# Performance work log

Hardware: AMD Instinct MI355X
Metric: run time of the kernel (lower is better)

## Reference

```python
import jax, jax.numpy as jnp
import numpy as np

B, N, ND_, FEAT, WV = 32, 1024, 8, 2048, 300
E, T, STEPS = 20000, 2, 5
NDIM = N * ND_  # 8192


def setup_inputs() -> dict:
    key = jax.random.key(0)
    ks = jax.random.split(key, 20)
    s = 0.02
    inputs = jax.random.normal(ks[0], (B, FEAT), jnp.float32)
    wordvecs = jax.random.normal(ks[1], (N, WV), jnp.float32)
    # unique edges per type (disjoint across types) so the scatter has no duplicate indices
    rng = np.random.default_rng(0)
    codes = rng.permutation(N * N)[: T * E].reshape(T, E)
    edge_u = (codes // N).astype(np.int32)
    edge_v = (codes % N).astype(np.int32)
    ki = np.repeat(np.arange(ND_), ND_)
    kj = np.tile(np.arange(ND_), ND_)
    mat_u = (edge_u.reshape(-1)[:, None] * ND_ + ki[None, :]).reshape(-1).astype(np.int32)
    mat_v = (edge_v.reshape(-1)[:, None] * ND_ + kj[None, :]).reshape(-1).astype(np.int32)
    p = {
        'inputs': inputs, 'wordvecs': wordvecs,
        'edge_u': jnp.asarray(edge_u), 'edge_v': jnp.asarray(edge_v),
        'mat_u': jnp.asarray(mat_u), 'mat_v': jnp.asarray(mat_v),
        # Inputnet: Linear(feat+wv -> 512), Linear(512 -> node_dim)
        'W_in1': jax.random.normal(ks[2], (512, FEAT + WV), jnp.float32) * s,
        'b_in1': jnp.zeros((512,), jnp.float32),
        'W_in2': jax.random.normal(ks[3], (ND_, 512), jnp.float32) * s,
        'b_in2': jnp.zeros((ND_,), jnp.float32),
        # embnet: Linear(wv -> 50)
        'W_emb': jax.random.normal(ks[4], (50, WV), jnp.float32) * s,
        'b_emb': jnp.zeros((50,), jnp.float32),
        # relnets: one (50, 50*nd^2) matrix per edge type
        'rel_mats': jax.random.normal(ks[5], (T, 50, 50 * ND_ * ND_), jnp.float32) * s,
        # GRUCell(node_dim, node_dim)
        'W_ih': jax.random.normal(ks[6], (3 * ND_, ND_), jnp.float32) * s,
        'W_hh': jax.random.normal(ks[7], (3 * ND_, ND_), jnp.float32) * s,
        'b_ih': jnp.zeros((3 * ND_,), jnp.float32),
        'b_hh': jnp.zeros((3 * ND_,), jnp.float32),
        # outnet: Linear(nd -> 20), ReLU, Linear(20 -> 1)
        'W_o1': jax.random.normal(ks[8], (20, ND_), jnp.float32) * s,
        'b_o1': jnp.zeros((20,), jnp.float32),
        'W_o2': jax.random.normal(ks[9], (1, 20), jnp.float32) * s,
        'b_o2': jnp.zeros((1,), jnp.float32),
    }
    return p


def reference(inputs, wordvecs, edge_u, edge_v, mat_u, mat_v,
              W_in1, b_in1, W_in2, b_in2, W_emb, b_emb, rel_mats,
              W_ih, W_hh, b_ih, b_hh, W_o1, b_o1, W_o2, b_o2):
    nd = W_in2.shape[0]
    n_nodes = wordvecs.shape[0]
    ndim = n_nodes * nd
    bsz = inputs.shape[0]

    # Inputnet: per-(image, node) feature -> initial hidden state [B, N*nd]
    f = jnp.concatenate([
        jnp.broadcast_to(inputs[:, None, :], (bsz, n_nodes, inputs.shape[1])),
        jnp.broadcast_to(wordvecs[None, :, :], (bsz, n_nodes, wordvecs.shape[1])),
    ], axis=-1).reshape(bsz * n_nodes, -1)
    h = jax.nn.relu(f @ W_in1.T + b_in1) @ W_in2.T + b_in2  # [B*N, nd]
    hidden = h.reshape(bsz, ndim)

    # edge weights via Relnet per edge type
    embs = wordvecs @ W_emb.T + b_emb  # [N, 50]
    ws = []
    for t in range(rel_mats.shape[0]):
        ue = embs[edge_u[t]]  # [E, 50]
        ve = embs[edge_v[t]]  # [E, 50]
        tmp = (ue @ rel_mats[t]).reshape(ue.shape[0], embs.shape[1], nd * nd)
        ws.append(jnp.einsum('ed,edk->ek', ve, tmp))  # [E, nd^2]
    weights = jnp.concatenate(ws, axis=0).reshape(-1)

    # scatter into dense propagation matrix
    P = jnp.zeros((ndim, ndim), jnp.float32).at[mat_u, mat_v].set(weights)
    norm = jnp.sqrt(jnp.sum(P * P, axis=1))  # row L2 norms [ndim]
    norm = norm + (norm == 0).astype(P.dtype)
    P = P / norm  # NOTE: torch broadcasting divides COLUMNS by row norms (faithful)

    def gru(x, hc):
        gi = x @ W_ih.T + b_ih
        gh = hc @ W_hh.T + b_hh
        ir, iz, inn = jnp.split(gi, 3, axis=-1)
        hr, hz, hn = jnp.split(gh, 3, axis=-1)
        r = jax.nn.sigmoid(ir + hr)
        z = jax.nn.sigmoid(iz + hz)
        n = jnp.tanh(inn + r * hn)
        return (1.0 - z) * n + z * hc

    hiddens = [hidden]
    for _ in range(STEPS):
        x = jnp.tanh(hidden @ P.T)  # [B, ndim]
        hidden = gru(x.reshape(-1, nd), hidden.reshape(-1, nd)).reshape(bsz, ndim)
        hiddens.append(hidden)
    states = jnp.stack(hiddens, axis=1)  # [B, STEPS+1, ndim]

    o = jax.nn.relu(states.reshape(-1, nd) @ W_o1.T + b_o1) @ W_o2.T + b_o2  # [B*(S+1)*N, 1]
    logits = o.reshape(bsz, STEPS + 1, n_nodes).transpose(0, 2, 1)  # [B, N, S+1]
    return logits
```

## Files before the change

kernel.cpp:

```cpp
#include <hip/hip_runtime.h>
#include <math.h>

constexpr int B = 32, N = 1024, ND = 8, FEAT = 2048, WVD = 300;
constexpr int E = 20000, T = 2, STEPS = 5;
constexpr int NDIM = N * ND;
constexpr int H1 = 512;
constexpr int W1C = FEAT + WVD;
constexpr int EMB = 50;
constexpr int RC = EMB * ND * ND;
constexpr int SEG = 16;
constexpr int SEGLEN = E / SEG;

constexpr int G_KA   = 512;
constexpr int G_W1T  = 16 * 10;
constexpr int G_EMB  = N * EMB / 4;
constexpr int G_SEGH = T * N * SEG / 4;
constexpr int F1_TOT = G_KA + G_W1T + G_EMB + G_SEGH;

constexpr int G_ARED = 8;
constexpr int G_WV2  = 256;
constexpr int G_AHAT = 13 * (N / 32) * T;
constexpr int F2_TOT = 1 + G_ARED + G_WV2 + G_AHAT;

constexpr int F4_TOT = 2 * N;

__global__ __launch_bounds__(256) void k_f1(
        const int* eu, int* segcnt,
        const float* inp, const float* W1, float* partA, float* W1T,
        const float* wv, const float* We, const float* be,
        float* embs, float* embsT) {
    __shared__ float smem[8 * 260];
    int tid = threadIdx.x;
    int blk = blockIdx.x;
    if (blk < G_KA) {
        int c = tid & 7, b = tid >> 3;
        int c0 = (blk & 63) * 8;
        int ks = blk >> 6;
        int kt = ks * 256;
        {
            int r = tid >> 5, cb = (tid & 31) * 8;
            const float* src = W1 + (size_t)(c0 + r) * W1C + kt + cb;
            float4 a0 = *(const float4*)src;
            float4 a1 = *(const float4*)(src + 4);
            *(float4*)&smem[r * 260 + cb] = a0;
            *(float4*)&smem[r * 260 + cb + 4] = a1;
        }
        __syncthreads();
        const float* xr = inp + (size_t)b * FEAT + kt;
        float acc = 0.f;
#pragma unroll 8
        for (int k4 = 0; k4 < 64; k4++) {
            float4 x = *(const float4*)(xr + k4 * 4);
            float4 w = *(const float4*)&smem[c * 260 + k4 * 4];
            acc += x.x * w.x + x.y * w.y + x.z * w.z + x.w * w.w;
        }
        partA[(size_t)ks * (H1 * B) + (c0 + c) * B + b] = acc;
    } else if (blk < G_KA + G_W1T) {
        int lb = blk - G_KA;
        int c0 = (lb % 16) * 32, k0 = (lb / 16) * 32;
        float (*tile)[33] = (float(*)[33])smem;
        int kl = tid & 31, cl4 = tid >> 5;
#pragma unroll
        for (int p = 0; p < 4; p++) {
            int c = cl4 + p * 8;
            int k = k0 + kl;
            if (k < WVD) tile[c][kl] = W1[(size_t)(c0 + c) * W1C + FEAT + k];
        }
        __syncthreads();
        int cl = tid & 31, kl4 = tid >> 5;
#pragma unroll
        for (int p = 0; p < 4; p++) {
            int kk = kl4 + p * 8;
            int k = k0 + kk;
            if (k < WVD) W1T[(size_t)k * H1 + c0 + cl] = tile[cl][kk];
        }
    } else if (blk < G_KA + G_W1T + G_EMB) {
        int lb = blk - G_KA - G_W1T;
        int wid = lb * 4 + (tid >> 6);
        int lane = tid & 63;
        int n = wid / EMB, c = wid - n * EMB;
        const float* xr = wv + (size_t)n * WVD;
        const float* wr = We + (size_t)c * WVD;
        float acc = 0.f;
#pragma unroll
        for (int i = 0; i < 5; i++) {
            int k = i * 64 + lane;
            if (k < WVD) acc += xr[k] * wr[k];
        }
        for (int m = 32; m; m >>= 1) acc += __shfl_xor(acc, m, 64);
        if (lane == 0) {
            float v = acc + be[c];
            embs[n * EMB + c] = v;
            embsT[c * N + n] = v;
        }
    } else {
        int lb = blk - G_KA - G_W1T - G_EMB;
        int wid = lb * 4 + (tid >> 6);
        int lane = tid & 63;
        int t = wid >> 14, u = (wid >> 4) & (N - 1), seg = wid & (SEG - 1);
        const int* eut = eu + t * E;
        int e0 = seg * SEGLEN, e1 = e0 + SEGLEN, cnt = 0;
        for (int c = e0; c < e1; c += 64) {
            int e = c + lane;
            bool ok = (e < e1) && (eut[e] == u);
            cnt += __popcll(__ballot(ok));
        }
        if (lane == 0) segcnt[wid] = cnt;
    }
}

__global__ __launch_bounds__(256) void k_f2(
        const int* segcnt, int* segoff, int* counts, int* ptr,
        const float* partA, float* AbT,
        const float* wv, const float* W1T, float* Wvb,
        const float* embsT, const float* RMbase, float* Ahat) {
    __shared__ float smemf[4096];
    int tid = threadIdx.x, blk = blockIdx.x;
    if (blk == 0) {
        int* sc = (int*)smemf;
        for (int row = tid; row < 2048; row += 256) {
            int acc = 0;
            const int* src = segcnt + row * SEG;
            int* dst = segoff + row * SEG;
#pragma unroll
            for (int s = 0; s < SEG; s++) { dst[s] = acc; acc += src[s]; }
            counts[row] = acc;
            sc[row] = acc;
        }
        __syncthreads();
        int* src = sc; int* dst = sc + 2048;
        for (int st = 1; st < 2048; st <<= 1) {
            for (int j = tid; j < 2048; j += 256)
                dst[j] = src[j] + (j >= st ? src[j - st] : 0);
            __syncthreads();
            int* tmp = src; src = dst; dst = tmp;
        }
        for (int j = tid; j < 2048; j += 256)
            ptr[j] = j ? src[j - 1] : 0;
    } else if (blk <= G_ARED) {
        int cb = (blk - 1) * 2048 + tid * 8;
        if (cb < H1 * B) {
            float4 s0 = {0, 0, 0, 0}, s1 = {0, 0, 0, 0};
#pragma unroll
            for (int ks = 0; ks < 8; ks++) {
                const float* p = partA + (size_t)ks * (H1 * B) + cb;
                float4 a = *(const float4*)p;
                float4 b4 = *(const float4*)(p + 4);
                s0.x += a.x; s0.y += a.y; s0.z += a.z; s0.w += a.w;
                s1.x += b4.x; s1.y += b4.y; s1.z += b4.z; s1.w += b4.w;
            }
            *(float4*)(AbT + cb) = s0;
            *(float4*)(AbT + cb + 4) = s1;
        }
    } else if (blk <= G_ARED + G_WV2) {
        int lb = blk - 1 - G_ARED;
        int c = (lb & 1) * 256 + tid;
        int n0 = (lb >> 1) * 8;
        float (*el)[WVD] = (float(*)[WVD])smemf;
        for (int idx = tid; idx < 8 * WVD; idx += 256)
            el[idx / WVD][idx % WVD] = wv[(size_t)(n0 + idx / WVD) * WVD + idx % WVD];
        __syncthreads();
        float acc[8] = {};
        for (int k = 0; k < WVD; k++) {
            float r = W1T[(size_t)k * H1 + c];
#pragma unroll
            for (int j = 0; j < 8; j++) acc[j] += el[j][k] * r;
        }
#pragma unroll
        for (int j = 0; j < 8; j++) Wvb[(size_t)(n0 + j) * H1 + c] = acc[j];
    } else {
        int lb = blk - 1 - G_ARED - G_WV2;
        int t = lb / (13 * 32), r = lb % (13 * 32);
        int bx = r % 13, by = r / 13;
        const float* RM = RMbase + (size_t)t * EMB * RC;
        float* Ah = Ahat + (size_t)t * N * RC;
        int n0 = by * 32;
        float (*el)[36] = (float(*)[36])smemf;
        for (int idx = tid; idx < EMB * 32; idx += 256)
            el[idx >> 5][idx & 31] = embsT[(idx >> 5) * N + n0 + (idx & 31)];
        __syncthreads();
        int mi = bx * 256 + (tid & 63) * 4;
        int ni = (tid >> 6) * 8;
        if (mi < RC) {
            float acc[8][4] = {};
            for (int c = 0; c < EMB; c++) {
                float4 rm = *(const float4*)(RM + (size_t)c * RC + mi);
                float4 e0 = *(const float4*)&el[c][ni];
                float4 e1 = *(const float4*)&el[c][ni + 4];
                float ev[8] = {e0.x, e0.y, e0.z, e0.w, e1.x, e1.y, e1.z, e1.w};
#pragma unroll
                for (int j = 0; j < 8; j++) {
                    acc[j][0] += ev[j] * rm.x;
                    acc[j][1] += ev[j] * rm.y;
                    acc[j][2] += ev[j] * rm.z;
                    acc[j][3] += ev[j] * rm.w;
                }
            }
#pragma unroll
            for (int j = 0; j < 8; j++) {
                float4 o = {acc[j][0], acc[j][1], acc[j][2], acc[j][3]};
                *(float4*)(Ah + (size_t)(n0 + ni + j) * RC + mi) = o;
            }
        }
    }
}

__global__ __launch_bounds__(256) void k_f3(
        const int* eu, const int* ev, const int* ptr, const int* segoff, int* sv) {
    int tid = threadIdx.x, blk = blockIdx.x;
    int wid = blk * 4 + (tid >> 6);
    int lane = tid & 63;
    int t = wid >> 14, u = (wid >> 4) & (N - 1), seg = wid & (SEG - 1);
    const int* eut = eu + t * E;
    const int* evt = ev + t * E;
    int row = t * N + u;
    int base = ptr[row] + segoff[row * SEG + seg];
    int e0 = seg * SEGLEN, e1 = e0 + SEGLEN, cnt = 0;
    for (int c = e0; c < e1; c += 64) {
        int e = c + lane;
        bool ok = (e < e1) && (eut[e] == u);
        unsigned long long m = __ballot(ok);
        if (ok) {
            int rank = __popcll(m & ((1ull << lane) - 1));
            sv[base + cnt + rank] = evt[e];
        }
        cnt += __popcll(m);
    }
}

__global__ __launch_bounds__(256) void k_f4(
        const int* ptr, const int* counts, const int* sv,
        const float* embs, const float* Ahat, float* wbuf, float* inorm,
        const float* AbT, const float* Wvb, const float* b1,
        const float* W2, const float* b2, float* sT0) {
    __shared__ float smem[6656];
    int tid = threadIdx.x;
    int blk = blockIdx.x;
    if (blk < N) {
        float* AL = smem;
        int u = blk;
        int wv_ = tid >> 6, k = tid & 63;
        float ssq = 0.f;
        for (int t = 0; t < T; t++) {
            __syncthreads();
            for (int idx = tid; idx < RC; idx += 256)
                AL[idx] = Ahat[((size_t)t * N + u) * RC + idx];
            __syncthreads();
            int base = ptr[t * N + u], cnt = counts[t * N + u];
            for (int i = wv_; i < cnt; i += 4) {
                int slot = base + i;
                int v = sv[slot];
                const float* vr = embs + v * EMB;
                float acc = 0.f;
#pragma unroll 10
                for (int d = 0; d < EMB; d++) acc += vr[d] * AL[d * 64 + k];
                wbuf[(size_t)slot * 64 + k] = acc;
                ssq += acc * acc;
            }
        }
        __syncthreads();
        AL[wv_ * 64 + k] = ssq;
        __syncthreads();
        if (tid < 64) {
            float tot = AL[tid] + AL[64 + tid] + AL[128 + tid] + AL[192 + tid];
            tot += __shfl_xor(tot, 1, 64);
            tot += __shfl_xor(tot, 2, 64);
            tot += __shfl_xor(tot, 4, 64);
            int ki = tid >> 3, kj = tid & 7;
            if (kj == 0) {
                float nv = sqrtf(tot);
                if (nv == 0.f) nv = 1.f;
                inorm[u * ND + ki] = 1.0f / nv;
            }
        }
    } else {
        int n = blk - N;
        float* w2s  = smem;
        float* wvs  = smem + 4096;
        float* part = smem + 4608;
        for (int idx = tid; idx < 8 * H1; idx += 256) w2s[idx] = W2[idx];
        for (int idx = tid; idx < H1; idx += 256)
            wvs[idx] = Wvb[(size_t)n * H1 + idx] + b1[idx];
        __syncthreads();
        int b = tid & 31, s = tid >> 5;
        float acc[8] = {};
        for (int i = 0; i < 64; i++) {
            int c = s * 64 + i;
            float tv = fmaxf(AbT[c * 32 + b] + wvs[c], 0.f);
#pragma unroll
            for (int ki = 0; ki < 8; ki++) acc[ki] += tv * w2s[ki * H1 + c];
        }
#pragma unroll
        for (int ki = 0; ki < 8; ki++) part[s * 256 + ki * 32 + b] = acc[ki];
        __syncthreads();
        int ki2 = tid >> 5, b2i = tid & 31;
        float tot = b2[ki2];
#pragma unroll
        for (int s2 = 0; s2 < 8; s2++) tot += part[s2 * 256 + ki2 * 32 + b2i];
        sT0[(size_t)n * 256 + tid] = tot;
    }
}

__global__ __launch_bounds__(256) void k_step(
        const int* ptr, const int* counts, const int* sv,
        const float* wbuf, const float* inorm, const float* sT, int s,
        const float* W_ih, const float* W_hh, const float* b_ih, const float* b_hh,
        const float* Wo1, const float* bo1, const float* Wo2, const float* bo2,
        float* sOut, float* out, int last) {
    __shared__ float xs[256], hs[256], hfin[256];
    __shared__ float wih[192], whh[192];
    __shared__ float w1s[160], b1s[20], w2s[20];
    __shared__ float res[8][33];
    int tid = threadIdx.x;
    int u = blockIdx.x;
    int ki = tid >> 5, b = tid & 31;
    if (tid < 192) { wih[tid] = W_ih[tid]; whh[tid] = W_hh[tid]; }
    if (last) {
        if (tid < 160) w1s[tid] = Wo1[tid];
        if (tid < 20) { b1s[tid] = bo1[tid]; w2s[tid] = Wo2[tid]; }
    }
    const float* sIn = sT + (size_t)s * NDIM * B;
    float hown = sIn[((size_t)u * 8 + ki) * B + b];
    float acc = 0.f;
    for (int t = 0; t < T; t++) {
        int base = ptr[t * N + u], cnt = counts[t * N + u];
        for (int i = 0; i < cnt; i++) {
            int slot = base + i;
            int v = sv[slot];
            const float* wp = wbuf + (size_t)slot * 64 + ki * 8;
            float4 wa = *(const float4*)wp;
            float4 wb = *(const float4*)(wp + 4);
            const float* ip = inorm + v * ND;
            const float* hp = sIn + (size_t)v * 256 + b;
            acc += (wa.x * ip[0]) * hp[0]
                 + (wa.y * ip[1]) * hp[32]
                 + (wa.z * ip[2]) * hp[64]
                 + (wa.w * ip[3]) * hp[96]
                 + (wb.x * ip[4]) * hp[128]
                 + (wb.y * ip[5]) * hp[160]
                 + (wb.z * ip[6]) * hp[192]
                 + (wb.w * ip[7]) * hp[224];
        }
    }
    float xv = tanhf(acc);
    xs[ki * 32 + b] = xv;
    hs[ki * 32 + b] = hown;
    __syncthreads();
    float gr = b_ih[ki], gz = b_ih[8 + ki], gn = b_ih[16 + ki];
    float hr = b_hh[ki], hz = b_hh[8 + ki], hn = b_hh[16 + ki];
#pragma unroll
    for (int j = 0; j < 8; j++) {
        float xj = xs[j * 32 + b], hj = hs[j * 32 + b];
        gr += wih[ki * 8 + j] * xj;
        gz += wih[(8 + ki) * 8 + j] * xj;
        gn += wih[(16 + ki) * 8 + j] * xj;
        hr += whh[ki * 8 + j] * hj;
        hz += whh[(8 + ki) * 8 + j] * hj;
        hn += whh[(16 + ki) * 8 + j] * hj;
    }
    float r = 1.f / (1.f + expf(-(gr + hr)));
    float z = 1.f / (1.f + expf(-(gz + hz)));
    float nn = tanhf(gn + r * hn);
    float hnew = (1.f - z) * nn + z * hown;
    if (!last) {
        sOut[((size_t)u * 8 + ki) * B + b] = hnew;
        return;
    }
    hfin[ki * 32 + b] = hnew;
    __syncthreads();
    int s6 = tid >> 5, bb = tid & 31;
    if (s6 < 6) {
        float x[8];
#pragma unroll
        for (int kk = 0; kk < 8; kk++)
            x[kk] = (s6 < STEPS)
                ? sT[((size_t)s6 * NDIM + u * 8 + kk) * B + bb]
                : hfin[kk * 32 + bb];
        float accv = bo2[0];
#pragma unroll
        for (int j = 0; j < 20; j++) {
            float h = b1s[j];
#pragma unroll
            for (int kk = 0; kk < 8; kk++) h += w1s[j * 8 + kk] * x[kk];
            h = fmaxf(h, 0.f);
            accv += w2s[j] * h;
        }
        res[s6][bb] = accv;
    }
    __syncthreads();
    if (tid < 192) {
        int b_w = tid / 6, s_w = tid - b_w * 6;
        out[(size_t)b_w * ((STEPS + 1) * N) + u * (STEPS + 1) + s_w] = res[s_w][b_w];
    }
}

extern "C" void kernel_launch(void* const* d_in, const int* in_sizes, int n_in,
                              void* d_out, int out_size, void* d_ws, size_t ws_size,
                              hipStream_t stream) {
    const float* inputs   = (const float*)d_in[0];
    const float* wordvecs = (const float*)d_in[1];
    const int*   edge_u   = (const int*)d_in[2];
    const int*   edge_v   = (const int*)d_in[3];
    const float* W_in1 = (const float*)d_in[6];
    const float* b_in1 = (const float*)d_in[7];
    const float* W_in2 = (const float*)d_in[8];
    const float* b_in2 = (const float*)d_in[9];
    const float* W_emb = (const float*)d_in[10];
    const float* b_emb = (const float*)d_in[11];
    const float* rel_mats = (const float*)d_in[12];
    const float* W_ih = (const float*)d_in[13];
    const float* W_hh = (const float*)d_in[14];
    const float* b_ih = (const float*)d_in[15];
    const float* b_hh = (const float*)d_in[16];
    const float* W_o1 = (const float*)d_in[17];
    const float* b_o1 = (const float*)d_in[18];
    const float* W_o2 = (const float*)d_in[19];
    const float* b_o2 = (const float*)d_in[20];
    float* out = (float*)d_out;

    char* ws = (char*)d_ws;
    size_t off = 0;
    auto alloc = [&](size_t bytes) -> void* {
        void* p = ws + off;
        off = (off + bytes + 255) & ~(size_t)255;
        return p;
    };
    int* segcnt    = (int*)alloc((size_t)T * N * SEG * 4);
    int* segoff    = (int*)alloc((size_t)T * N * SEG * 4);
    int* counts    = (int*)alloc(2048 * 4);
    int* ptr       = (int*)alloc(2048 * 4);
    int* sv        = (int*)alloc((size_t)T * E * 4);
    float* inorm   = (float*)alloc((size_t)NDIM * 4);
    float* partA   = (float*)alloc((size_t)8 * H1 * B * 4);
    float* AbT     = (float*)alloc((size_t)H1 * B * 4);
    float* W1T     = (float*)alloc((size_t)WVD * H1 * 4);
    float* Wvb     = (float*)alloc((size_t)N * H1 * 4);
    float* embs    = (float*)alloc((size_t)N * EMB * 4);
    float* embsT   = (float*)alloc((size_t)EMB * N * 4);
    float* Ahat    = (float*)alloc((size_t)T * N * RC * 4);
    float* wbuf    = (float*)alloc((size_t)T * E * 64 * 4);
    float* sT      = (float*)alloc((size_t)(STEPS + 1) * NDIM * B * 4);

    k_f1<<<F1_TOT, 256, 0, stream>>>(edge_u, segcnt, inputs, W_in1, partA, W1T,
                                     wordvecs, W_emb, b_emb, embs, embsT);
    k_f2<<<F2_TOT, 256, 0, stream>>>(segcnt, segoff, counts, ptr,
                                     partA, AbT,
                                     wordvecs, W1T, Wvb, embsT, rel_mats, Ahat);
    k_f3<<<T * N * SEG / 4, 256, 0, stream>>>(edge_u, edge_v, ptr, segoff, sv);
    k_f4<<<F4_TOT, 256, 0, stream>>>(ptr, counts, sv, embs, Ahat, wbuf, inorm,
                                     AbT, Wvb, b_in1, W_in2, b_in2, sT);

    for (int s = 0; s < STEPS; s++) {
        int last = (s == STEPS - 1) ? 1 : 0;
        k_step<<<N, 256, 0, stream>>>(ptr, counts, sv, wbuf, inorm, sT, s,
                                      W_ih, W_hh, b_ih, b_hh,
                                      W_o1, b_o1, W_o2, b_o2,
                                      sT + (size_t)(s + 1) * NDIM * B, out, last);
    }
}
```

Baseline: 274.9 us.

## Prescale edge weights by column norms, split K in word-vector GEMM, unroll loops

Adds a kernel that multiplies each stored edge weight by its column's inverse norm once, so the per-step propagation loop no longer loads and multiplies inorm. The step loop is also unrolled by two edges to expose more memory-level parallelism. The word-vector projection GEMM is split into two K halves across twice as many blocks, and the two partial results are summed when read. The embedding dot products are computed two outputs per wavefront, and an unroll pragma is added to the Ahat GEMM. The extra launch and the additional partial buffer cost some overhead and memory traffic.

```diff
diff --git a/kernel.cpp b/kernel.cpp
--- a/kernel.cpp
+++ b/kernel.cpp
@@ -10,15 +10,16 @@
 constexpr int RC = EMB * ND * ND;
 constexpr int SEG = 16;
 constexpr int SEGLEN = E / SEG;
+constexpr int KH = 150;
 
 constexpr int G_KA   = 512;
 constexpr int G_W1T  = 16 * 10;
-constexpr int G_EMB  = N * EMB / 4;
+constexpr int G_EMB  = N * 25 / 4;
 constexpr int G_SEGH = T * N * SEG / 4;
 constexpr int F1_TOT = G_KA + G_W1T + G_EMB + G_SEGH;
 
 constexpr int G_ARED = 8;
-constexpr int G_WV2  = 256;
+constexpr int G_WV2  = 512;
 constexpr int G_AHAT = 13 * (N / 32) * T;
 constexpr int F2_TOT = 1 + G_ARED + G_WV2 + G_AHAT;
 
@@ -78,20 +79,31 @@
         int lb = blk - G_KA - G_W1T;
         int wid = lb * 4 + (tid >> 6);
         int lane = tid & 63;
-        int n = wid / EMB, c = wid - n * EMB;
+        int n = wid / 25, cp = wid - n * 25;
+        int c0 = cp * 2;
         const float* xr = wv + (size_t)n * WVD;
-        const float* wr = We + (size_t)c * WVD;
-        float acc = 0.f;
+        const float* wr0 = We + (size_t)c0 * WVD;
+        const float* wr1 = wr0 + WVD;
+        float a0 = 0.f, a1 = 0.f;
 #pragma unroll
         for (int i = 0; i < 5; i++) {
             int k = i * 64 + lane;
-            if (k < WVD) acc += xr[k] * wr[k];
-        }
-        for (int m = 32; m; m >>= 1) acc += __shfl_xor(acc, m, 64);
+            if (k < WVD) {
+                float x = xr[k];
+                a0 += x * wr0[k];
+                a1 += x * wr1[k];
+            }
+        }
+        for (int m = 32; m; m >>= 1) {
+            a0 += __shfl_xor(a0, m, 64);
+            a1 += __shfl_xor(a1, m, 64);
+        }
         if (lane == 0) {
-            float v = acc + be[c];
-            embs[n * EMB + c] = v;
-            embsT[c * N + n] = v;
+            float v0 = a0 + be[c0], v1 = a1 + be[c0 + 1];
+            embs[n * EMB + c0] = v0;
+            embs[n * EMB + c0 + 1] = v1;
+            embsT[c0 * N + n] = v0;
+            embsT[(c0 + 1) * N + n] = v1;
         }
     } else {
         int lb = blk - G_KA - G_W1T - G_EMB;
@@ -112,7 +124,7 @@
 __global__ __launch_bounds__(256) void k_f2(
         const int* segcnt, int* segoff, int* counts, int* ptr,
         const float* partA, float* AbT,
-        const float* wv, const float* W1T, float* Wvb,
+        const float* wv, const float* W1T, float* Wp,
         const float* embsT, const float* RMbase, float* Ahat) {
     __shared__ float smemf[4096];
     int tid = threadIdx.x, blk = blockIdx.x;
@@ -154,20 +166,27 @@
         }
     } else if (blk <= G_ARED + G_WV2) {
         int lb = blk - 1 - G_ARED;
-        int c = (lb & 1) * 256 + tid;
-        int n0 = (lb >> 1) * 8;
-        float (*el)[WVD] = (float(*)[WVD])smemf;
-        for (int idx = tid; idx < 8 * WVD; idx += 256)
-            el[idx / WVD][idx % WVD] = wv[(size_t)(n0 + idx / WVD) * WVD + idx % WVD];
+        int kh = lb >> 8;
+        int rem = lb & 255;
+        int c = (rem & 1) * 256 + tid;
+        int n0 = (rem >> 1) * 8;
+        int kb = kh * KH;
+        float (*el)[152] = (float(*)[152])smemf;
+        for (int idx = tid; idx < 8 * KH; idx += 256) {
+            int j = idx / KH, k = idx - j * KH;
+            el[j][k] = wv[(size_t)(n0 + j) * WVD + kb + k];
+        }
         __syncthreads();
         float acc[8] = {};
-        for (int k = 0; k < WVD; k++) {
-            float r = W1T[(size_t)k * H1 + c];
+#pragma unroll 5
+        for (int k = 0; k < KH; k++) {
+            float r = W1T[(size_t)(kb + k) * H1 + c];
 #pragma unroll
             for (int j = 0; j < 8; j++) acc[j] += el[j][k] * r;
         }
-#pragma unroll
-        for (int j = 0; j < 8; j++) Wvb[(size_t)(n0 + j) * H1 + c] = acc[j];
+        float* wout = Wp + (size_t)kh * N * H1;
+#pragma unroll
+        for (int j = 0; j < 8; j++) wout[(size_t)(n0 + j) * H1 + c] = acc[j];
     } else {
         int lb = blk - 1 - G_ARED - G_WV2;
         int t = lb / (13 * 32), r = lb % (13 * 32);
@@ -183,6 +202,7 @@
         int ni = (tid >> 6) * 8;
         if (mi < RC) {
             float acc[8][4] = {};
+#pragma unroll 2
             for (int c = 0; c < EMB; c++) {
                 float4 rm = *(const float4*)(RM + (size_t)c * RC + mi);
                 float4 e0 = *(const float4*)&el[c][ni];
@@ -231,7 +251,7 @@
 __global__ __launch_bounds__(256) void k_f4(
         const int* ptr, const int* counts, const int* sv,
         const float* embs, const float* Ahat, float* wbuf, float* inorm,
-        const float* AbT, const float* Wvb, const float* b1,
+        const float* AbT, const float* Wp, const float* b1,
         const float* W2, const float* b2, float* sT0) {
     __shared__ float smem[6656];
     int tid = threadIdx.x;
@@ -280,7 +300,8 @@
         float* part = smem + 4608;
         for (int idx = tid; idx < 8 * H1; idx += 256) w2s[idx] = W2[idx];
         for (int idx = tid; idx < H1; idx += 256)
-            wvs[idx] = Wvb[(size_t)n * H1 + idx] + b1[idx];
+            wvs[idx] = Wp[(size_t)n * H1 + idx]
+                     + Wp[(size_t)N * H1 + (size_t)n * H1 + idx] + b1[idx];
         __syncthreads();
         int b = tid & 31, s = tid >> 5;
         float acc[8] = {};
@@ -301,9 +322,17 @@
     }
 }
 
+__global__ __launch_bounds__(256) void k_sc(const int* sv, float* wbuf,
+                                            const float* inorm) {
+    int idx = blockIdx.x * 256 + threadIdx.x;
+    int slot = idx >> 6, k = idx & 63;
+    int v = sv[slot];
+    wbuf[idx] = wbuf[idx] * inorm[v * ND + (k & 7)];
+}
+
 __global__ __launch_bounds__(256) void k_step(
         const int* ptr, const int* counts, const int* sv,
-        const float* wbuf, const float* inorm, const float* sT, int s,
+        const float* wbuf, const float* sT, int s,
         const float* W_ih, const float* W_hh, const float* b_ih, const float* b_hh,
         const float* Wo1, const float* bo1, const float* Wo2, const float* bo2,
         float* sOut, float* out, int last) {
@@ -324,22 +353,32 @@
     float acc = 0.f;
     for (int t = 0; t < T; t++) {
         int base = ptr[t * N + u], cnt = counts[t * N + u];
-        for (int i = 0; i < cnt; i++) {
-            int slot = base + i;
-            int v = sv[slot];
-            const float* wp = wbuf + (size_t)slot * 64 + ki * 8;
-            float4 wa = *(const float4*)wp;
-            float4 wb = *(const float4*)(wp + 4);
-            const float* ip = inorm + v * ND;
-            const float* hp = sIn + (size_t)v * 256 + b;
-            acc += (wa.x * ip[0]) * hp[0]
-                 + (wa.y * ip[1]) * hp[32]
-                 + (wa.z * ip[2]) * hp[64]
-                 + (wa.w * ip[3]) * hp[96]
-                 + (wb.x * ip[4]) * hp[128]
-                 + (wb.y * ip[5]) * hp[160]
-                 + (wb.z * ip[6]) * hp[192]
-                 + (wb.w * ip[7]) * hp[224];
+        int i = 0;
+        for (; i + 1 < cnt; i += 2) {
+            int s0 = base + i, s1 = base + i + 1;
+            int v0 = sv[s0], v1 = sv[s1];
+            const float* wp0 = wbuf + (size_t)s0 * 64 + ki * 8;
+            const float* wp1 = wbuf + (size_t)s1 * 64 + ki * 8;
+            float4 wa0 = *(const float4*)wp0;
+            float4 wb0 = *(const float4*)(wp0 + 4);
+            float4 wa1 = *(const float4*)wp1;
+            float4 wb1 = *(const float4*)(wp1 + 4);
+            const float* hp0 = sIn + (size_t)v0 * 256 + b;
+            const float* hp1 = sIn + (size_t)v1 * 256 + b;
+            acc += wa0.x * hp0[0]   + wa0.y * hp0[32]  + wa0.z * hp0[64]  + wa0.w * hp0[96]
+                 + wb0.x * hp0[128] + wb0.y * hp0[160] + wb0.z * hp0[192] + wb0.w * hp0[224];
+            acc += wa1.x * hp1[0]   + wa1.y * hp1[32]  + wa1.z * hp1[64]  + wa1.w * hp1[96]
+                 + wb1.x * hp1[128] + wb1.y * hp1[160] + wb1.z * hp1[192] + wb1.w * hp1[224];
+        }
+        if (i < cnt) {
+            int s0 = base + i;
+            int v0 = sv[s0];
+            const float* wp0 = wbuf + (size_t)s0 * 64 + ki * 8;
+            float4 wa0 = *(const float4*)wp0;
+            float4 wb0 = *(const float4*)(wp0 + 4);
+            const float* hp0 = sIn + (size_t)v0 * 256 + b;
+            acc += wa0.x * hp0[0]   + wa0.y * hp0[32]  + wa0.z * hp0[64]  + wa0.w * hp0[96]
+                 + wb0.x * hp0[128] + wb0.y * hp0[160] + wb0.z * hp0[192] + wb0.w * hp0[224];
         }
     }
     float xv = tanhf(acc);
@@ -434,7 +473,7 @@
     float* partA   = (float*)alloc((size_t)8 * H1 * B * 4);
     float* AbT     = (float*)alloc((size_t)H1 * B * 4);
     float* W1T     = (float*)alloc((size_t)WVD * H1 * 4);
-    float* Wvb     = (float*)alloc((size_t)N * H1 * 4);
+    float* Wp      = (float*)alloc((size_t)2 * N * H1 * 4);
     float* embs    = (float*)alloc((size_t)N * EMB * 4);
     float* embsT   = (float*)alloc((size_t)EMB * N * 4);
     float* Ahat    = (float*)alloc((size_t)T * N * RC * 4);
@@ -445,14 +484,15 @@
                                      wordvecs, W_emb, b_emb, embs, embsT);
     k_f2<<<F2_TOT, 256, 0, stream>>>(segcnt, segoff, counts, ptr,
                                      partA, AbT,
-                                     wordvecs, W1T, Wvb, embsT, rel_mats, Ahat);
+                                     wordvecs, W1T, Wp, embsT, rel_mats, Ahat);
     k_f3<<<T * N * SEG / 4, 256, 0, stream>>>(edge_u, edge_v, ptr, segoff, sv);
     k_f4<<<F4_TOT, 256, 0, stream>>>(ptr, counts, sv, embs, Ahat, wbuf, inorm,
-                                     AbT, Wvb, b_in1, W_in2, b_in2, sT);
+                                     AbT, Wp, b_in1, W_in2, b_in2, sT);
+    k_sc<<<T * E * 64 / 256, 256, 0, stream>>>(sv, wbuf, inorm);
 
     for (int s = 0; s < STEPS; s++) {
         int last = (s == STEPS - 1) ? 1 : 0;
-        k_step<<<N, 256, 0, stream>>>(ptr, counts, sv, wbuf, inorm, sT, s,
+        k_step<<<N, 256, 0, stream>>>(ptr, counts, sv, wbuf, sT, s,
                                       W_ih, W_hh, b_ih, b_hh,
                                       W_o1, b_o1, W_o2, b_o2,
                                       sT + (size_t)(s + 1) * NDIM * B, out, last);
```

New measurement: 276.0 us. About the same (+0.4%).
